# Kernel tuning notes

Hardware: AMD Instinct MI355X
Metric: run time of the kernel (lower is better)

The kernel has to match this reference:

```python
import jax, jax.numpy as jnp
import numpy as np

N_NODES = 100000
N_EDGES = 1600000
N_CONCEPTS = 500000
D = 128  # concept_dim = graph_hidden_dim = graph_output_dim


def setup_inputs() -> dict:
    key = jax.random.key(0)
    ks = jax.random.split(key, 10)
    cncpt_ids = jax.random.randint(ks[0], (N_NODES,), 0, N_CONCEPTS)
    src = jax.random.randint(ks[1], (N_EDGES,), 0, N_NODES)
    dst = jax.random.randint(ks[2], (N_EDGES,), 0, N_NODES)
    emb_table = jax.random.normal(ks[3], (N_CONCEPTS, D), dtype=jnp.float32)
    W1 = jax.random.normal(ks[4], (D, D), dtype=jnp.float32) * 0.05
    b1 = jax.random.normal(ks[5], (D,), dtype=jnp.float32) * 0.05
    W2 = jax.random.normal(ks[6], (D, D), dtype=jnp.float32) * 0.05
    b2 = jax.random.normal(ks[7], (D,), dtype=jnp.float32) * 0.05
    Wout = jax.random.normal(ks[8], (1, D), dtype=jnp.float32) * 0.05
    bout = jax.random.normal(ks[9], (1,), dtype=jnp.float32) * 0.05
    return {"cncpt_ids": cncpt_ids, "src": src, "dst": dst,
            "emb_table": emb_table, "W1": W1, "b1": b1,
            "W2": W2, "b2": b2, "Wout": Wout, "bout": bout}


def _gcn_layer(h, src, dst, W, b, n_nodes):
    # DGL update_all(copy_src, sum): gather messages from src, sum into dst
    agg = jax.ops.segment_sum(h[src], dst, num_segments=n_nodes)  # [N, d_in]
    return jax.nn.relu(agg @ W.T + b)  # NodeApplyModule: Linear + ReLU


def reference(cncpt_ids, src, dst, emb_table, W1, b1, W2, b2, Wout, bout):
    n_nodes = cncpt_ids.shape[0]
    h = emb_table[cncpt_ids]                       # [N, D] concept embeddings
    h = _gcn_layer(h, src, dst, W1, b1, n_nodes)   # gcn1
    h = _gcn_layer(h, src, dst, W2, b2, n_nodes)   # gcn2
    x = h[None]                                    # torch.stack([h]) -> [1, N, D]
    logits = jax.nn.sigmoid(x @ Wout.T + bout)     # hidden2output -> [1, N, 1]
    return logits
```

## Files before the change

### kernel.cpp

```cpp
#include <hip/hip_runtime.h>
#include <math.h>

#define D 128
#define SCAN_B 256

typedef __attribute__((ext_vector_type(8))) short bfrag;
typedef __attribute__((ext_vector_type(4))) float ffrag;

__device__ inline unsigned short f2bf(float f) {
    unsigned u = __float_as_uint(f);
    u += 0x7FFF + ((u >> 16) & 1);
    return (unsigned short)(u >> 16);
}
__device__ inline float bf2f(unsigned short h) {
    return __uint_as_float(((unsigned)h) << 16);
}
__device__ inline unsigned pack_bf2(float a, float b) {
    return ((unsigned)f2bf(a)) | (((unsigned)f2bf(b)) << 16);
}

__global__ void zero_int_kernel(int* __restrict__ buf, int n) {
    int i = blockIdx.x * blockDim.x + threadIdx.x;
    if (i < n) buf[i] = 0;
}

__global__ void wsplit_kernel(const float* __restrict__ W1,
                              const float* __restrict__ W2,
                              unsigned short* __restrict__ hi1,
                              unsigned short* __restrict__ lo1,
                              unsigned short* __restrict__ hi2,
                              unsigned short* __restrict__ lo2, int n) {
    int i = blockIdx.x * blockDim.x + threadIdx.x;
    if (i >= n) return;
    float f1 = W1[i];
    unsigned short h1 = f2bf(f1);
    hi1[i] = h1;
    lo1[i] = f2bf(f1 - bf2f(h1));
    float f2 = W2[i];
    unsigned short h2 = f2bf(f2);
    hi2[i] = h2;
    lo2[i] = f2bf(f2 - bf2f(h2));
}

__global__ void gather_kernel(const float* __restrict__ emb,
                              const int* __restrict__ ids,
                              uint4* __restrict__ h4, int n_nodes) {
    int idx = blockIdx.x * blockDim.x + threadIdx.x;
    int total = n_nodes * 16;
    if (idx >= total) return;
    int node = idx >> 4;
    int c = idx & 15;
    size_t cid = (size_t)ids[node];
    const float4* s = (const float4*)(emb + cid * D) + c * 2;
    float4 v0 = s[0];
    float4 v1 = s[1];
    uint4 p;
    p.x = pack_bf2(v0.x, v0.y);
    p.y = pack_bf2(v0.z, v0.w);
    p.z = pack_bf2(v1.x, v1.y);
    p.w = pack_bf2(v1.z, v1.w);
    h4[(size_t)node * 16 + c] = p;
}

__global__ void degree_kernel(const int* __restrict__ dst,
                              int* __restrict__ deg, int n_edges) {
    int e = blockIdx.x * blockDim.x + threadIdx.x;
    if (e < n_edges) atomicAdd(&deg[dst[e]], 1);
}

__global__ __launch_bounds__(SCAN_B) void scan_block_kernel(
        const int* __restrict__ deg, int* __restrict__ row_ptr,
        int* __restrict__ blocksums, int n) {
    __shared__ int s[SCAN_B];
    int i = blockIdx.x * SCAN_B + threadIdx.x;
    int v = (i < n) ? deg[i] : 0;
    s[threadIdx.x] = v;
    __syncthreads();
    #pragma unroll
    for (int off = 1; off < SCAN_B; off <<= 1) {
        int t = (threadIdx.x >= off) ? s[threadIdx.x - off] : 0;
        __syncthreads();
        s[threadIdx.x] += t;
        __syncthreads();
    }
    if (i < n) row_ptr[i] = s[threadIdx.x] - v;
    if (threadIdx.x == SCAN_B - 1) blocksums[blockIdx.x] = s[SCAN_B - 1];
}

__global__ __launch_bounds__(512) void scan_sums_kernel(int* __restrict__ blocksums,
                                                        int nb) {
    __shared__ int s[512];
    int v = (threadIdx.x < nb) ? blocksums[threadIdx.x] : 0;
    s[threadIdx.x] = v;
    __syncthreads();
    #pragma unroll
    for (int off = 1; off < 512; off <<= 1) {
        int t = (threadIdx.x >= off) ? s[threadIdx.x - off] : 0;
        __syncthreads();
        s[threadIdx.x] += t;
        __syncthreads();
    }
    if (threadIdx.x < nb) blocksums[threadIdx.x] = s[threadIdx.x] - v;
}

__global__ void add_offsets_kernel(int* __restrict__ row_ptr,
                                   const int* __restrict__ blocksums,
                                   int* __restrict__ cursor, int n, int n_nodes) {
    int i = blockIdx.x * blockDim.x + threadIdx.x;
    if (i >= n) return;
    int rp = row_ptr[i] + blocksums[i / SCAN_B];
    row_ptr[i] = rp;
    if (i < n_nodes) cursor[i] = rp;
}

__global__ void csr_fill_kernel(const int* __restrict__ src,
                                const int* __restrict__ dst,
                                int* __restrict__ cursor,
                                int* __restrict__ esrc, int n_edges) {
    int e = blockIdx.x * blockDim.x + threadIdx.x;
    if (e >= n_edges) return;
    int pos = atomicAdd(&cursor[dst[e]], 1);
    esrc[pos] = src[e];
}

__global__ __launch_bounds__(256) void agg_kernel(
        const uint4* __restrict__ h4, const int* __restrict__ row_ptr,
        const int* __restrict__ esrc, uint4* __restrict__ agg4, int n_nodes) {
    int node = blockIdx.x * 4 + (threadIdx.x >> 6);
    int lane = threadIdx.x & 63;
    if (node >= n_nodes) return;
    const int c = lane & 15;
    const int g = lane >> 4;
    int beg = row_ptr[node], end = row_ptr[node + 1];

    float a0 = 0.f, a1 = 0.f, a2 = 0.f, a3 = 0.f;
    float a4 = 0.f, a5 = 0.f, a6 = 0.f, a7 = 0.f;

    int i = beg + g;
    for (; i + 4 < end; i += 8) {
        int s0 = esrc[i];
        int s1 = esrc[i + 4];
        uint4 u0 = h4[(size_t)s0 * 16 + c];
        uint4 u1 = h4[(size_t)s1 * 16 + c];
        a0 += __uint_as_float(u0.x << 16) + __uint_as_float(u1.x << 16);
        a1 += __uint_as_float(u0.x & 0xffff0000u) + __uint_as_float(u1.x & 0xffff0000u);
        a2 += __uint_as_float(u0.y << 16) + __uint_as_float(u1.y << 16);
        a3 += __uint_as_float(u0.y & 0xffff0000u) + __uint_as_float(u1.y & 0xffff0000u);
        a4 += __uint_as_float(u0.z << 16) + __uint_as_float(u1.z << 16);
        a5 += __uint_as_float(u0.z & 0xffff0000u) + __uint_as_float(u1.z & 0xffff0000u);
        a6 += __uint_as_float(u0.w << 16) + __uint_as_float(u1.w << 16);
        a7 += __uint_as_float(u0.w & 0xffff0000u) + __uint_as_float(u1.w & 0xffff0000u);
    }
    if (i < end) {
        uint4 u = h4[(size_t)esrc[i] * 16 + c];
        a0 += __uint_as_float(u.x << 16);
        a1 += __uint_as_float(u.x & 0xffff0000u);
        a2 += __uint_as_float(u.y << 16);
        a3 += __uint_as_float(u.y & 0xffff0000u);
        a4 += __uint_as_float(u.z << 16);
        a5 += __uint_as_float(u.z & 0xffff0000u);
        a6 += __uint_as_float(u.w << 16);
        a7 += __uint_as_float(u.w & 0xffff0000u);
    }

    a0 += __shfl_xor(a0, 16, 64); a0 += __shfl_xor(a0, 32, 64);
    a1 += __shfl_xor(a1, 16, 64); a1 += __shfl_xor(a1, 32, 64);
    a2 += __shfl_xor(a2, 16, 64); a2 += __shfl_xor(a2, 32, 64);
    a3 += __shfl_xor(a3, 16, 64); a3 += __shfl_xor(a3, 32, 64);
    a4 += __shfl_xor(a4, 16, 64); a4 += __shfl_xor(a4, 32, 64);
    a5 += __shfl_xor(a5, 16, 64); a5 += __shfl_xor(a5, 32, 64);
    a6 += __shfl_xor(a6, 16, 64); a6 += __shfl_xor(a6, 32, 64);
    a7 += __shfl_xor(a7, 16, 64); a7 += __shfl_xor(a7, 32, 64);

    if (g == 0) {
        uint4 r;
        r.x = pack_bf2(a0, a1);
        r.y = pack_bf2(a2, a3);
        r.z = pack_bf2(a4, a5);
        r.w = pack_bf2(a6, a7);
        agg4[(size_t)node * 16 + c] = r;
    }
}

__global__ __launch_bounds__(256) void linear_mfma_kernel(
        const unsigned short* __restrict__ x,
        const unsigned short* __restrict__ Whi,
        const unsigned short* __restrict__ Wlo,
        const float* __restrict__ b,
        unsigned short* __restrict__ y,
        const float* __restrict__ wout,
        const float* __restrict__ bout,
        float* __restrict__ outp,
        int n_nodes, int fuse_out) {
    const int lane = threadIdx.x & 63;
    const int col  = lane & 15;
    const int quad = lane >> 4;
    const int wave = blockIdx.x * 4 + (threadIdx.x >> 6);
    const int nwaves = gridDim.x * 4;
    const int ngroups = (n_nodes + 15) >> 4;

    float bvals[8], wvals[8];
    #pragma unroll
    for (int nt = 0; nt < 8; ++nt) {
        bvals[nt] = b[nt * 16 + col];
        wvals[nt] = fuse_out ? wout[nt * 16 + col] : 0.f;
    }
    const float bout0 = fuse_out ? bout[0] : 0.f;

    for (int g = wave; g < ngroups; g += nwaves) {
        int node = g * 16 + col;
        int nload = node < n_nodes ? node : (n_nodes - 1);

        bfrag a[4];
        #pragma unroll
        for (int kt = 0; kt < 4; ++kt)
            a[kt] = *(const bfrag*)(x + (size_t)nload * D + kt * 32 + quad * 8);

        const size_t bbase = (size_t)col * D + quad * 8;
        float part0 = 0.f, part1 = 0.f, part2 = 0.f, part3 = 0.f;

        #pragma unroll
        for (int nt = 0; nt < 8; ++nt) {
            ffrag c = {0.f, 0.f, 0.f, 0.f};
            #pragma unroll
            for (int kt = 0; kt < 4; ++kt) {
                size_t off = (size_t)nt * 16 * D + bbase + kt * 32;
                bfrag bh = *(const bfrag*)(Whi + off);
                bfrag bl = *(const bfrag*)(Wlo + off);
                c = __builtin_amdgcn_mfma_f32_16x16x32_bf16(a[kt], bh, c, 0, 0, 0);
                c = __builtin_amdgcn_mfma_f32_16x16x32_bf16(a[kt], bl, c, 0, 0, 0);
            }
            if (fuse_out) {
                part0 += fmaxf(c[0] + bvals[nt], 0.f) * wvals[nt];
                part1 += fmaxf(c[1] + bvals[nt], 0.f) * wvals[nt];
                part2 += fmaxf(c[2] + bvals[nt], 0.f) * wvals[nt];
                part3 += fmaxf(c[3] + bvals[nt], 0.f) * wvals[nt];
            } else {
                #pragma unroll
                for (int r = 0; r < 4; ++r) {
                    int onode = g * 16 + quad * 4 + r;
                    if (onode < n_nodes)
                        y[(size_t)onode * D + nt * 16 + col] =
                            f2bf(fmaxf(c[r] + bvals[nt], 0.f));
                }
            }
        }

        if (fuse_out) {
            float part[4] = {part0, part1, part2, part3};
            #pragma unroll
            for (int r = 0; r < 4; ++r) {
                float s = part[r];
                s += __shfl_xor(s, 1, 64);
                s += __shfl_xor(s, 2, 64);
                s += __shfl_xor(s, 4, 64);
                s += __shfl_xor(s, 8, 64);
                int onode = g * 16 + quad * 4 + r;
                if (col == 0 && onode < n_nodes)
                    outp[onode] = 1.0f / (1.0f + expf(-(s + bout0)));
            }
        }
    }
}

extern "C" void kernel_launch(void* const* d_in, const int* in_sizes, int n_in,
                              void* d_out, int out_size, void* d_ws, size_t ws_size,
                              hipStream_t stream) {
    const int*   cncpt_ids = (const int*)d_in[0];
    const int*   src       = (const int*)d_in[1];
    const int*   dst       = (const int*)d_in[2];
    const float* emb       = (const float*)d_in[3];
    const float* W1        = (const float*)d_in[4];
    const float* b1        = (const float*)d_in[5];
    const float* W2        = (const float*)d_in[6];
    const float* b2        = (const float*)d_in[7];
    const float* Wout      = (const float*)d_in[8];
    const float* bout      = (const float*)d_in[9];
    float* out = (float*)d_out;

    const int n_nodes = in_sizes[0];
    const int n_edges = in_sizes[1];

    unsigned short* bufA = (unsigned short*)d_ws;
    unsigned short* bufB = bufA + (size_t)n_nodes * D;
    int*   deg      = (int*)(bufB + (size_t)n_nodes * D);
    int*   row_ptr  = deg + (n_nodes + 1);
    int*   cursor   = row_ptr + (n_nodes + 1);
    int*   blocksums= cursor + n_nodes;
    int*   esrc     = blocksums + 512;
    unsigned short* W1hi = (unsigned short*)(esrc + n_edges);
    unsigned short* W1lo = W1hi + D * D;
    unsigned short* W2hi = W1lo + D * D;
    unsigned short* W2lo = W2hi + D * D;

    const int np1 = n_nodes + 1;
    const int nb_scan = (np1 + SCAN_B - 1) / SCAN_B;

    wsplit_kernel<<<(D * D + 255) / 256, 256, 0, stream>>>(
        W1, W2, W1hi, W1lo, W2hi, W2lo, D * D);

    gather_kernel<<<(n_nodes * 16 + 255) / 256, 256, 0, stream>>>(
        emb, cncpt_ids, (uint4*)bufA, n_nodes);

    zero_int_kernel<<<(np1 + 255) / 256, 256, 0, stream>>>(deg, np1);
    degree_kernel<<<(n_edges + 255) / 256, 256, 0, stream>>>(dst, deg, n_edges);
    scan_block_kernel<<<nb_scan, SCAN_B, 0, stream>>>(deg, row_ptr, blocksums, np1);
    scan_sums_kernel<<<1, 512, 0, stream>>>(blocksums, nb_scan);
    add_offsets_kernel<<<(np1 + 255) / 256, 256, 0, stream>>>(
        row_ptr, blocksums, cursor, np1, n_nodes);
    csr_fill_kernel<<<(n_edges + 255) / 256, 256, 0, stream>>>(
        src, dst, cursor, esrc, n_edges);

    const int agg_grid = (n_nodes + 3) / 4;
    const int ngroups = (n_nodes + 15) / 16;
    const int lin_grid = (ngroups + 7) / 8;

    agg_kernel<<<agg_grid, 256, 0, stream>>>(
        (const uint4*)bufA, row_ptr, esrc, (uint4*)bufB, n_nodes);
    linear_mfma_kernel<<<lin_grid, 256, 0, stream>>>(
        bufB, W1hi, W1lo, b1, bufA, nullptr, nullptr, nullptr, n_nodes, 0);

    agg_kernel<<<agg_grid, 256, 0, stream>>>(
        (const uint4*)bufA, row_ptr, esrc, (uint4*)bufB, n_nodes);
    linear_mfma_kernel<<<lin_grid, 256, 0, stream>>>(
        bufB, W2hi, W2lo, b2, nullptr, Wout, bout, out, n_nodes, 1);
}
```

Measured before the change: 725.5 us.

## Fuse neighbor aggregation with MFMA linear layer via LDS staging

Merges the aggregation kernel and the linear MFMA kernel into one per-layer kernel. Each wave aggregates 16 nodes into a padded LDS tile, then feeds the MFMA from LDS, so the bf16 aggregate never round-trips through global memory. It also merges the weight split, embedding gather and degree zeroing into one init kernel to cut launches. In exchange, the aggregation now uses 16 lanes per node with a shallower per-node unroll instead of 64 lanes per node, which reduces memory-level parallelism per node and adds block-wide syncs.

```diff
diff --git a/kernel.cpp b/kernel.cpp
--- a/kernel.cpp
+++ b/kernel.cpp
@@ -19,47 +19,43 @@
     return ((unsigned)f2bf(a)) | (((unsigned)f2bf(b)) << 16);
 }
 
-__global__ void zero_int_kernel(int* __restrict__ buf, int n) {
-    int i = blockIdx.x * blockDim.x + threadIdx.x;
-    if (i < n) buf[i] = 0;
-}
-
-__global__ void wsplit_kernel(const float* __restrict__ W1,
-                              const float* __restrict__ W2,
-                              unsigned short* __restrict__ hi1,
-                              unsigned short* __restrict__ lo1,
-                              unsigned short* __restrict__ hi2,
-                              unsigned short* __restrict__ lo2, int n) {
-    int i = blockIdx.x * blockDim.x + threadIdx.x;
-    if (i >= n) return;
-    float f1 = W1[i];
-    unsigned short h1 = f2bf(f1);
-    hi1[i] = h1;
-    lo1[i] = f2bf(f1 - bf2f(h1));
-    float f2 = W2[i];
-    unsigned short h2 = f2bf(f2);
-    hi2[i] = h2;
-    lo2[i] = f2bf(f2 - bf2f(h2));
-}
-
-__global__ void gather_kernel(const float* __restrict__ emb,
-                              const int* __restrict__ ids,
-                              uint4* __restrict__ h4, int n_nodes) {
+__global__ void init_kernel(const float* __restrict__ emb,
+                            const int* __restrict__ ids,
+                            uint4* __restrict__ h4,
+                            const float* __restrict__ W1,
+                            const float* __restrict__ W2,
+                            unsigned short* __restrict__ hi1,
+                            unsigned short* __restrict__ lo1,
+                            unsigned short* __restrict__ hi2,
+                            unsigned short* __restrict__ lo2,
+                            int* __restrict__ deg,
+                            int n_nodes, int np1) {
     int idx = blockIdx.x * blockDim.x + threadIdx.x;
-    int total = n_nodes * 16;
-    if (idx >= total) return;
-    int node = idx >> 4;
-    int c = idx & 15;
-    size_t cid = (size_t)ids[node];
-    const float4* s = (const float4*)(emb + cid * D) + c * 2;
-    float4 v0 = s[0];
-    float4 v1 = s[1];
-    uint4 p;
-    p.x = pack_bf2(v0.x, v0.y);
-    p.y = pack_bf2(v0.z, v0.w);
-    p.z = pack_bf2(v1.x, v1.y);
-    p.w = pack_bf2(v1.z, v1.w);
-    h4[(size_t)node * 16 + c] = p;
+    if (idx < n_nodes * 16) {
+        int node = idx >> 4;
+        int c = idx & 15;
+        size_t cid = (size_t)ids[node];
+        const float4* s = (const float4*)(emb + cid * D) + c * 2;
+        float4 v0 = s[0];
+        float4 v1 = s[1];
+        uint4 p;
+        p.x = pack_bf2(v0.x, v0.y);
+        p.y = pack_bf2(v0.z, v0.w);
+        p.z = pack_bf2(v1.x, v1.y);
+        p.w = pack_bf2(v1.z, v1.w);
+        h4[(size_t)node * 16 + c] = p;
+    }
+    if (idx < D * D) {
+        float f1 = W1[idx];
+        unsigned short h1 = f2bf(f1);
+        hi1[idx] = h1;
+        lo1[idx] = f2bf(f1 - bf2f(h1));
+        float f2 = W2[idx];
+        unsigned short h2 = f2bf(f2);
+        hi2[idx] = h2;
+        lo2[idx] = f2bf(f2 - bf2f(h2));
+    }
+    if (idx < np1) deg[idx] = 0;
 }
 
 __global__ void degree_kernel(const int* __restrict__ dst,
@@ -123,67 +119,10 @@
     esrc[pos] = src[e];
 }
 
-__global__ __launch_bounds__(256) void agg_kernel(
-        const uint4* __restrict__ h4, const int* __restrict__ row_ptr,
-        const int* __restrict__ esrc, uint4* __restrict__ agg4, int n_nodes) {
-    int node = blockIdx.x * 4 + (threadIdx.x >> 6);
-    int lane = threadIdx.x & 63;
-    if (node >= n_nodes) return;
-    const int c = lane & 15;
-    const int g = lane >> 4;
-    int beg = row_ptr[node], end = row_ptr[node + 1];
-
-    float a0 = 0.f, a1 = 0.f, a2 = 0.f, a3 = 0.f;
-    float a4 = 0.f, a5 = 0.f, a6 = 0.f, a7 = 0.f;
-
-    int i = beg + g;
-    for (; i + 4 < end; i += 8) {
-        int s0 = esrc[i];
-        int s1 = esrc[i + 4];
-        uint4 u0 = h4[(size_t)s0 * 16 + c];
-        uint4 u1 = h4[(size_t)s1 * 16 + c];
-        a0 += __uint_as_float(u0.x << 16) + __uint_as_float(u1.x << 16);
-        a1 += __uint_as_float(u0.x & 0xffff0000u) + __uint_as_float(u1.x & 0xffff0000u);
-        a2 += __uint_as_float(u0.y << 16) + __uint_as_float(u1.y << 16);
-        a3 += __uint_as_float(u0.y & 0xffff0000u) + __uint_as_float(u1.y & 0xffff0000u);
-        a4 += __uint_as_float(u0.z << 16) + __uint_as_float(u1.z << 16);
-        a5 += __uint_as_float(u0.z & 0xffff0000u) + __uint_as_float(u1.z & 0xffff0000u);
-        a6 += __uint_as_float(u0.w << 16) + __uint_as_float(u1.w << 16);
-        a7 += __uint_as_float(u0.w & 0xffff0000u) + __uint_as_float(u1.w & 0xffff0000u);
-    }
-    if (i < end) {
-        uint4 u = h4[(size_t)esrc[i] * 16 + c];
-        a0 += __uint_as_float(u.x << 16);
-        a1 += __uint_as_float(u.x & 0xffff0000u);
-        a2 += __uint_as_float(u.y << 16);
-        a3 += __uint_as_float(u.y & 0xffff0000u);
-        a4 += __uint_as_float(u.z << 16);
-        a5 += __uint_as_float(u.z & 0xffff0000u);
-        a6 += __uint_as_float(u.w << 16);
-        a7 += __uint_as_float(u.w & 0xffff0000u);
-    }
-
-    a0 += __shfl_xor(a0, 16, 64); a0 += __shfl_xor(a0, 32, 64);
-    a1 += __shfl_xor(a1, 16, 64); a1 += __shfl_xor(a1, 32, 64);
-    a2 += __shfl_xor(a2, 16, 64); a2 += __shfl_xor(a2, 32, 64);
-    a3 += __shfl_xor(a3, 16, 64); a3 += __shfl_xor(a3, 32, 64);
-    a4 += __shfl_xor(a4, 16, 64); a4 += __shfl_xor(a4, 32, 64);
-    a5 += __shfl_xor(a5, 16, 64); a5 += __shfl_xor(a5, 32, 64);
-    a6 += __shfl_xor(a6, 16, 64); a6 += __shfl_xor(a6, 32, 64);
-    a7 += __shfl_xor(a7, 16, 64); a7 += __shfl_xor(a7, 32, 64);
-
-    if (g == 0) {
-        uint4 r;
-        r.x = pack_bf2(a0, a1);
-        r.y = pack_bf2(a2, a3);
-        r.z = pack_bf2(a4, a5);
-        r.w = pack_bf2(a6, a7);
-        agg4[(size_t)node * 16 + c] = r;
-    }
-}
-
-__global__ __launch_bounds__(256) void linear_mfma_kernel(
-        const unsigned short* __restrict__ x,
+__global__ __launch_bounds__(256) void gcn_layer_kernel(
+        const uint4* __restrict__ h4,
+        const int* __restrict__ row_ptr,
+        const int* __restrict__ esrc,
         const unsigned short* __restrict__ Whi,
         const unsigned short* __restrict__ Wlo,
         const float* __restrict__ b,
@@ -192,61 +131,110 @@
         const float* __restrict__ bout,
         float* __restrict__ outp,
         int n_nodes, int fuse_out) {
+    __shared__ unsigned short lds[4][16 * 136];
+    const int wv   = threadIdx.x >> 6;
     const int lane = threadIdx.x & 63;
-    const int col  = lane & 15;
-    const int quad = lane >> 4;
-    const int wave = blockIdx.x * 4 + (threadIdx.x >> 6);
+    const int c    = lane & 15;
+    const int gid  = lane >> 4;
+    const int wave = blockIdx.x * 4 + wv;
     const int nwaves = gridDim.x * 4;
     const int ngroups = (n_nodes + 15) >> 4;
+    const int iters = (ngroups + nwaves - 1) / nwaves;
 
     float bvals[8], wvals[8];
     #pragma unroll
     for (int nt = 0; nt < 8; ++nt) {
-        bvals[nt] = b[nt * 16 + col];
-        wvals[nt] = fuse_out ? wout[nt * 16 + col] : 0.f;
+        bvals[nt] = b[nt * 16 + c];
+        wvals[nt] = fuse_out ? wout[nt * 16 + c] : 0.f;
     }
     const float bout0 = fuse_out ? bout[0] : 0.f;
 
-    for (int g = wave; g < ngroups; g += nwaves) {
-        int node = g * 16 + col;
-        int nload = node < n_nodes ? node : (n_nodes - 1);
+    for (int it = 0; it < iters; ++it) {
+        int g = wave + it * nwaves;
+        bool active = g < ngroups;
+
+        #pragma unroll
+        for (int pass = 0; pass < 4; ++pass) {
+            int node = g * 16 + pass * 4 + gid;
+            int beg = 0, end = 0;
+            if (active && node < n_nodes) {
+                beg = row_ptr[node];
+                end = row_ptr[node + 1];
+            }
+            float a0 = 0.f, a1 = 0.f, a2 = 0.f, a3 = 0.f;
+            float a4 = 0.f, a5 = 0.f, a6 = 0.f, a7 = 0.f;
+            int i = beg;
+            for (; i + 1 < end; i += 2) {
+                int s0 = esrc[i];
+                int s1 = esrc[i + 1];
+                uint4 u0 = h4[(size_t)s0 * 16 + c];
+                uint4 u1 = h4[(size_t)s1 * 16 + c];
+                a0 += __uint_as_float(u0.x << 16) + __uint_as_float(u1.x << 16);
+                a1 += __uint_as_float(u0.x & 0xffff0000u) + __uint_as_float(u1.x & 0xffff0000u);
+                a2 += __uint_as_float(u0.y << 16) + __uint_as_float(u1.y << 16);
+                a3 += __uint_as_float(u0.y & 0xffff0000u) + __uint_as_float(u1.y & 0xffff0000u);
+                a4 += __uint_as_float(u0.z << 16) + __uint_as_float(u1.z << 16);
+                a5 += __uint_as_float(u0.z & 0xffff0000u) + __uint_as_float(u1.z & 0xffff0000u);
+                a6 += __uint_as_float(u0.w << 16) + __uint_as_float(u1.w << 16);
+                a7 += __uint_as_float(u0.w & 0xffff0000u) + __uint_as_float(u1.w & 0xffff0000u);
+            }
+            if (i < end) {
+                uint4 u = h4[(size_t)esrc[i] * 16 + c];
+                a0 += __uint_as_float(u.x << 16);
+                a1 += __uint_as_float(u.x & 0xffff0000u);
+                a2 += __uint_as_float(u.y << 16);
+                a3 += __uint_as_float(u.y & 0xffff0000u);
+                a4 += __uint_as_float(u.z << 16);
+                a5 += __uint_as_float(u.z & 0xffff0000u);
+                a6 += __uint_as_float(u.w << 16);
+                a7 += __uint_as_float(u.w & 0xffff0000u);
+            }
+            int m = pass * 4 + gid;
+            uint4 p;
+            p.x = pack_bf2(a0, a1);
+            p.y = pack_bf2(a2, a3);
+            p.z = pack_bf2(a4, a5);
+            p.w = pack_bf2(a6, a7);
+            *(uint4*)&lds[wv][m * 136 + c * 8] = p;
+        }
+        __syncthreads();
 
         bfrag a[4];
         #pragma unroll
         for (int kt = 0; kt < 4; ++kt)
-            a[kt] = *(const bfrag*)(x + (size_t)nload * D + kt * 32 + quad * 8);
-
-        const size_t bbase = (size_t)col * D + quad * 8;
+            a[kt] = *(const bfrag*)&lds[wv][c * 136 + kt * 32 + gid * 8];
+
+        const size_t bbase = (size_t)c * D + gid * 8;
         float part0 = 0.f, part1 = 0.f, part2 = 0.f, part3 = 0.f;
 
         #pragma unroll
         for (int nt = 0; nt < 8; ++nt) {
-            ffrag c = {0.f, 0.f, 0.f, 0.f};
+            ffrag cc = {0.f, 0.f, 0.f, 0.f};
             #pragma unroll
             for (int kt = 0; kt < 4; ++kt) {
                 size_t off = (size_t)nt * 16 * D + bbase + kt * 32;
                 bfrag bh = *(const bfrag*)(Whi + off);
                 bfrag bl = *(const bfrag*)(Wlo + off);
-                c = __builtin_amdgcn_mfma_f32_16x16x32_bf16(a[kt], bh, c, 0, 0, 0);
-                c = __builtin_amdgcn_mfma_f32_16x16x32_bf16(a[kt], bl, c, 0, 0, 0);
+                cc = __builtin_amdgcn_mfma_f32_16x16x32_bf16(a[kt], bh, cc, 0, 0, 0);
+                cc = __builtin_amdgcn_mfma_f32_16x16x32_bf16(a[kt], bl, cc, 0, 0, 0);
             }
             if (fuse_out) {
-                part0 += fmaxf(c[0] + bvals[nt], 0.f) * wvals[nt];
-                part1 += fmaxf(c[1] + bvals[nt], 0.f) * wvals[nt];
-                part2 += fmaxf(c[2] + bvals[nt], 0.f) * wvals[nt];
-                part3 += fmaxf(c[3] + bvals[nt], 0.f) * wvals[nt];
-            } else {
+                part0 += fmaxf(cc[0] + bvals[nt], 0.f) * wvals[nt];
+                part1 += fmaxf(cc[1] + bvals[nt], 0.f) * wvals[nt];
+                part2 += fmaxf(cc[2] + bvals[nt], 0.f) * wvals[nt];
+                part3 += fmaxf(cc[3] + bvals[nt], 0.f) * wvals[nt];
+            } else if (active) {
                 #pragma unroll
                 for (int r = 0; r < 4; ++r) {
-                    int onode = g * 16 + quad * 4 + r;
+                    int onode = g * 16 + gid * 4 + r;
                     if (onode < n_nodes)
-                        y[(size_t)onode * D + nt * 16 + col] =
-                            f2bf(fmaxf(c[r] + bvals[nt], 0.f));
+                        y[(size_t)onode * D + nt * 16 + c] =
+                            f2bf(fmaxf(cc[r] + bvals[nt], 0.f));
                 }
             }
         }
 
-        if (fuse_out) {
+        if (fuse_out && active) {
             float part[4] = {part0, part1, part2, part3};
             #pragma unroll
             for (int r = 0; r < 4; ++r) {
@@ -255,11 +243,12 @@
                 s += __shfl_xor(s, 2, 64);
                 s += __shfl_xor(s, 4, 64);
                 s += __shfl_xor(s, 8, 64);
-                int onode = g * 16 + quad * 4 + r;
-                if (col == 0 && onode < n_nodes)
+                int onode = g * 16 + gid * 4 + r;
+                if (c == 0 && onode < n_nodes)
                     outp[onode] = 1.0f / (1.0f + expf(-(s + bout0)));
             }
         }
+        __syncthreads();
     }
 }
 
@@ -296,13 +285,10 @@
     const int np1 = n_nodes + 1;
     const int nb_scan = (np1 + SCAN_B - 1) / SCAN_B;
 
-    wsplit_kernel<<<(D * D + 255) / 256, 256, 0, stream>>>(
-        W1, W2, W1hi, W1lo, W2hi, W2lo, D * D);
-
-    gather_kernel<<<(n_nodes * 16 + 255) / 256, 256, 0, stream>>>(
-        emb, cncpt_ids, (uint4*)bufA, n_nodes);
-
-    zero_int_kernel<<<(np1 + 255) / 256, 256, 0, stream>>>(deg, np1);
+    init_kernel<<<(n_nodes * 16 + 255) / 256, 256, 0, stream>>>(
+        emb, cncpt_ids, (uint4*)bufA, W1, W2,
+        W1hi, W1lo, W2hi, W2lo, deg, n_nodes, np1);
+
     degree_kernel<<<(n_edges + 255) / 256, 256, 0, stream>>>(dst, deg, n_edges);
     scan_block_kernel<<<nb_scan, SCAN_B, 0, stream>>>(deg, row_ptr, blocksums, np1);
     scan_sums_kernel<<<1, 512, 0, stream>>>(blocksums, nb_scan);
@@ -311,17 +297,14 @@
     csr_fill_kernel<<<(n_edges + 255) / 256, 256, 0, stream>>>(
         src, dst, cursor, esrc, n_edges);
 
-    const int agg_grid = (n_nodes + 3) / 4;
     const int ngroups = (n_nodes + 15) / 16;
-    const int lin_grid = (ngroups + 7) / 8;
-
-    agg_kernel<<<agg_grid, 256, 0, stream>>>(
-        (const uint4*)bufA, row_ptr, esrc, (uint4*)bufB, n_nodes);
-    linear_mfma_kernel<<<lin_grid, 256, 0, stream>>>(
-        bufB, W1hi, W1lo, b1, bufA, nullptr, nullptr, nullptr, n_nodes, 0);
-
-    agg_kernel<<<agg_grid, 256, 0, stream>>>(
-        (const uint4*)bufA, row_ptr, esrc, (uint4*)bufB, n_nodes);
-    linear_mfma_kernel<<<lin_grid, 256, 0, stream>>>(
-        bufB, W2hi, W2lo, b2, nullptr, Wout, bout, out, n_nodes, 1);
-}
+    const int layer_grid = (ngroups + 3) / 4;
+
+    gcn_layer_kernel<<<layer_grid, 256, 0, stream>>>(
+        (const uint4*)bufA, row_ptr, esrc, W1hi, W1lo, b1,
+        bufB, nullptr, nullptr, nullptr, n_nodes, 0);
+
+    gcn_layer_kernel<<<layer_grid, 256, 0, stream>>>(
+        (const uint4*)bufB, row_ptr, esrc, W2hi, W2lo, b2,
+        nullptr, Wout, bout, out, n_nodes, 1);
+}
```

Measured after the change: 1.074 ms. 1.48x slower.
